# Performance work log

Hardware: AMD Instinct MI355X
Metric: run time of the kernel (lower is better)

The kernel has to match this reference:

```python
import jax, jax.numpy as jnp
import numpy as np

NUM_EXPERTS = 8
TOP_K = 2
D_MODEL = 1024
D_MLP = 3584
BATCH, POS = 2, 2048


def setup_inputs() -> dict:
    key = jax.random.key(0)
    ks = jax.random.split(key, 5)
    scale = 0.02
    x = jax.random.normal(ks[0], (BATCH, POS, D_MODEL), dtype=jnp.float32)
    W_gate = jax.random.normal(ks[1], (NUM_EXPERTS, D_MODEL), dtype=jnp.float32) * scale
    W1 = jax.random.normal(ks[2], (NUM_EXPERTS, D_MLP, D_MODEL), dtype=jnp.float32) * scale
    W3 = jax.random.normal(ks[3], (NUM_EXPERTS, D_MLP, D_MODEL), dtype=jnp.float32) * scale
    W2 = jax.random.normal(ks[4], (NUM_EXPERTS, D_MODEL, D_MLP), dtype=jnp.float32) * scale
    return {"x": x, "W_gate": W_gate, "W1": W1, "W3": W3, "W2": W2}


def reference(x, W_gate, W1, W3, W2):
    batch, pos, d_model = x.shape
    xt = x.reshape(-1, d_model)                      # [T, d]
    T = xt.shape[0]

    # --- top-2 softmax gating ---
    gate_logits = xt @ W_gate.T                      # [T, E]
    weights = jax.nn.softmax(gate_logits.astype(jnp.float32), axis=-1)
    top_w, top_i = jax.lax.top_k(weights, TOP_K)     # [T, k]
    top_w = top_w / jnp.sum(top_w, axis=-1, keepdims=True)
    top_w = top_w.astype(gate_logits.dtype)

    # dense combine weights: zero for non-selected experts  [T, E]
    combine = jnp.zeros((T, NUM_EXPERTS), dtype=xt.dtype)
    combine = combine.at[jnp.arange(T)[:, None], top_i].set(top_w)

    # --- per-expert SwiGLU MLP, computed dense over all tokens ---
    h1 = jnp.einsum('td,efd->etf', xt, W1)           # [E, T, ffn]
    h3 = jnp.einsum('td,efd->etf', xt, W3)           # [E, T, ffn]
    h = jax.nn.silu(h1) * h3                         # [E, T, ffn]
    expert_out = jnp.einsum('etf,edf->etd', h, W2)   # [E, T, d]

    # --- weighted combine ---
    out = jnp.einsum('etd,te->td', expert_out, combine)  # [T, d]
    return out.reshape(batch, pos, d_model)
```

## Files before the change

### kernel.cpp

```cpp
#include <hip/hip_runtime.h>
#include <hip/hip_bf16.h>
#include <math.h>


#define NUM_EXPERTS 8
#define TOPK 2
#define D_MODEL 1024
#define D_MLP 3584
#define T_TOKENS 4096
#define NSLOT (T_TOKENS * TOPK)
#define SLOT_CAP 9216

#define BM 128
#define BN 128
#define BK 32
#define LDT 40

typedef __attribute__((ext_vector_type(8))) short bf16x8;
typedef __attribute__((ext_vector_type(4))) float f32x4;

#define WS_SMALL 147456
#define H_BYTES ((size_t)SLOT_CAP * D_MLP * 2)
#define XB_OFF (WS_SMALL + H_BYTES)
#define XB_BYTES ((size_t)T_TOKENS * D_MODEL * 2)
#define W1B_OFF (XB_OFF + XB_BYTES)
#define W13_BYTES ((size_t)NUM_EXPERTS * (size_t)D_MLP * D_MODEL * 2)
#define W3B_OFF (W1B_OFF + W13_BYTES)
#define WS_FULL (W3B_OFF + W13_BYTES)
#define WS_NEEDED_OLD (WS_SMALL + H_BYTES)

__device__ inline unsigned short f32_to_bf16(float f) {
  union { float f; unsigned int u; } v; v.f = f;
  unsigned int u = v.u;
  unsigned int r = (u + 0x7FFFu + ((u >> 16) & 1u)) >> 16;
  return (unsigned short)r;
}

__device__ inline bf16x8 pack8(float4 a, float4 b) {
  bf16x8 v;
  v[0] = (short)f32_to_bf16(a.x); v[1] = (short)f32_to_bf16(a.y);
  v[2] = (short)f32_to_bf16(a.z); v[3] = (short)f32_to_bf16(a.w);
  v[4] = (short)f32_to_bf16(b.x); v[5] = (short)f32_to_bf16(b.y);
  v[6] = (short)f32_to_bf16(b.z); v[7] = (short)f32_to_bf16(b.w);
  return v;
}

__device__ __forceinline__ void gload16(const void* g, void* l) {
  __builtin_amdgcn_global_load_lds(
      (__attribute__((address_space(1))) void*)g,
      (__attribute__((address_space(3))) void*)l, 16, 0, 0);
}

__global__ void zero_kernel(float4* __restrict__ p, int n4) {
  int i = blockIdx.x * blockDim.x + threadIdx.x;
  if (i < n4) p[i] = make_float4(0.f, 0.f, 0.f, 0.f);
}

__global__ __launch_bounds__(256) void cvt_kernel(const float* __restrict__ src,
                                                  unsigned short* __restrict__ dst,
                                                  int n8) {
  int i = blockIdx.x * blockDim.x + threadIdx.x;
  const int stride = gridDim.x * blockDim.x;
  for (; i < n8; i += stride) {
    const float4* s = (const float4*)(src + (size_t)i * 8);
    float4 a = s[0], b = s[1];
    *(bf16x8*)(dst + (size_t)i * 8) = pack8(a, b);
  }
}

__global__ __launch_bounds__(64) void gate_kernel(const float* __restrict__ x,
                            const float* __restrict__ Wg,
                            int* __restrict__ top_idx,
                            float* __restrict__ top_w) {
  const int t = blockIdx.x;
  const int lane = threadIdx.x;
  const float* xr = x + (size_t)t * D_MODEL;

  float xs[16];
#pragma unroll
  for (int i = 0; i < 16; ++i) xs[i] = xr[lane + i * 64];

  float logits[NUM_EXPERTS];
#pragma unroll
  for (int e = 0; e < NUM_EXPERTS; ++e) {
    const float* wr = Wg + (size_t)e * D_MODEL;
    float s = 0.f;
#pragma unroll
    for (int i = 0; i < 16; ++i) s += xs[i] * wr[lane + i * 64];
    for (int o = 32; o > 0; o >>= 1) s += __shfl_down(s, o);
    logits[e] = s;
  }

  if (lane == 0) {
    int i0 = 0;
#pragma unroll
    for (int e = 1; e < NUM_EXPERTS; ++e)
      if (logits[e] > logits[i0]) i0 = e;
    int i1 = -1;
#pragma unroll
    for (int e = 0; e < NUM_EXPERTS; ++e) {
      if (e == i0) continue;
      if (i1 < 0 || logits[e] > logits[i1]) i1 = e;
    }
    float w0 = 1.0f / (1.0f + expf(logits[i1] - logits[i0]));
    top_idx[2 * t] = i0; top_idx[2 * t + 1] = i1;
    top_w[2 * t] = w0;   top_w[2 * t + 1] = 1.0f - w0;
  }
}

__global__ __launch_bounds__(256) void route_kernel(int* __restrict__ top_idx,
                             const float* __restrict__ top_w,
                             int* __restrict__ hdr,
                             int* __restrict__ slot_token,
                             float* __restrict__ slot_weight) {
  __shared__ int cnt[NUM_EXPERTS];
  __shared__ int off[NUM_EXPERTS];
  __shared__ int cur[NUM_EXPERTS];
  const int tid = threadIdx.x;
  if (tid < NUM_EXPERTS) cnt[tid] = 0;
  __syncthreads();
  for (int k = tid; k < NSLOT; k += 256) atomicAdd(&cnt[top_idx[k]], 1);
  __syncthreads();
  if (tid == 0) {
    int o = 0;
    for (int e = 0; e < NUM_EXPERTS; ++e) {
      off[e] = o;
      int p = (cnt[e] + BM - 1) & ~(BM - 1);
      hdr[e] = cnt[e];
      hdr[8 + e] = o;
      hdr[16 + e] = p;
      o += p;
    }
  }
  __syncthreads();
  if (tid < NUM_EXPERTS) cur[tid] = off[tid];
  for (int i = tid; i < SLOT_CAP; i += 256) { slot_token[i] = 0; slot_weight[i] = 0.0f; }
  __syncthreads();
  for (int k = tid; k < NSLOT; k += 256) {
    int e = top_idx[k];
    int p = atomicAdd(&cur[e], 1);
    slot_token[p] = k >> 1;
    slot_weight[p] = top_w[k];
    top_idx[k] = p;
  }
}

__global__ __launch_bounds__(256) void gemm1_p(
    const unsigned short* __restrict__ Xb,
    const unsigned short* __restrict__ W1b,
    const unsigned short* __restrict__ W3b,
    const int* __restrict__ hdr,
    const int* __restrict__ slot_token,
    unsigned short* __restrict__ H) {
  const int e = blockIdx.z;
  const int pad_cnt = hdr[16 + e];
  const int m0 = blockIdx.y * BM;
  if (m0 >= pad_cnt) return;
  const int base = hdr[8 + e];
  const int n0 = blockIdx.x * BN;

  __shared__ unsigned short As[2][BM * BK];
  __shared__ unsigned short B1s[2][BN * BK];
  __shared__ unsigned short B3s[2][BN * BK];

  const int tid = threadIdx.x;
  const int lane = tid & 63;
  const int wave = tid >> 6;
  const int wm = (wave >> 1) * 64;
  const int wn = (wave & 1) * 64;
  const int l15 = lane & 15;
  const int quad = lane >> 4;

  const int r0 = tid >> 2;
  const int cc = (tid & 3) * 8;
  const int tokA0 = slot_token[base + m0 + r0];
  const int tokA1 = slot_token[base + m0 + 64 + r0];
  const unsigned short* gA0 = Xb + (size_t)tokA0 * D_MODEL + cc;
  const unsigned short* gA1 = Xb + (size_t)tokA1 * D_MODEL + cc;
  const unsigned short* gB1_0 = W1b + ((size_t)e * D_MLP + n0 + r0) * D_MODEL + cc;
  const unsigned short* gB1_1 = gB1_0 + (size_t)64 * D_MODEL;
  const unsigned short* gB3_0 = W3b + ((size_t)e * D_MLP + n0 + r0) * D_MODEL + cc;
  const unsigned short* gB3_1 = gB3_0 + (size_t)64 * D_MODEL;
  const int wb = wave * 512;

  const f32x4 fzero = {0.f, 0.f, 0.f, 0.f};
  f32x4 acc1[4][4], acc3[4][4];
#pragma unroll
  for (int i = 0; i < 4; ++i)
#pragma unroll
    for (int j = 0; j < 4; ++j) { acc1[i][j] = fzero; acc3[i][j] = fzero; }

#define NT1 (D_MODEL / BK)
  gload16(gA0, &As[0][wb]);
  gload16(gA1, &As[0][2048 + wb]);
  gload16(gB1_0, &B1s[0][wb]);
  gload16(gB1_1, &B1s[0][2048 + wb]);
  gload16(gB3_0, &B3s[0][wb]);
  gload16(gB3_1, &B3s[0][2048 + wb]);

#pragma unroll
  for (int t = 0; t < NT1; ++t) {
    const int p = t & 1;
    if (t + 1 < NT1) {
      const int q = (t + 1) & 1;
      const int k1 = (t + 1) * BK;
      gload16(gA0 + k1, &As[q][wb]);
      gload16(gA1 + k1, &As[q][2048 + wb]);
      gload16(gB1_0 + k1, &B1s[q][wb]);
      gload16(gB1_1 + k1, &B1s[q][2048 + wb]);
      gload16(gB3_0 + k1, &B3s[q][wb]);
      gload16(gB3_1 + k1, &B3s[q][2048 + wb]);
      asm volatile("s_waitcnt vmcnt(6)" ::: "memory");
    } else {
      asm volatile("s_waitcnt vmcnt(0)" ::: "memory");
    }
    __builtin_amdgcn_s_barrier();
    asm volatile("" ::: "memory");

    bf16x8 af[4], b1f[4], b3f[4];
#pragma unroll
    for (int i = 0; i < 4; ++i)
      af[i] = *(const bf16x8*)(&As[p][(wm + i * 16 + l15) * BK + quad * 8]);
#pragma unroll
    for (int j = 0; j < 4; ++j) {
      b1f[j] = *(const bf16x8*)(&B1s[p][(wn + j * 16 + l15) * BK + quad * 8]);
      b3f[j] = *(const bf16x8*)(&B3s[p][(wn + j * 16 + l15) * BK + quad * 8]);
    }
#pragma unroll
    for (int i = 0; i < 4; ++i)
#pragma unroll
      for (int j = 0; j < 4; ++j) {
        acc1[i][j] = __builtin_amdgcn_mfma_f32_16x16x32_bf16(af[i], b1f[j], acc1[i][j], 0, 0, 0);
        acc3[i][j] = __builtin_amdgcn_mfma_f32_16x16x32_bf16(af[i], b3f[j], acc3[i][j], 0, 0, 0);
      }
    asm volatile("" ::: "memory");
    __builtin_amdgcn_s_barrier();
  }

  const size_t hbase = (size_t)(base + m0);
#pragma unroll
  for (int i = 0; i < 4; ++i) {
    const int mrow = wm + i * 16 + quad * 4;
#pragma unroll
    for (int r = 0; r < 4; ++r) {
      unsigned short* hrow = H + (hbase + mrow + r) * D_MLP + n0;
#pragma unroll
      for (int j = 0; j < 4; ++j) {
        float h1 = acc1[i][j][r];
        float h3 = acc3[i][j][r];
        float s = h1 / (1.0f + __expf(-h1));
        hrow[wn + j * 16 + l15] = f32_to_bf16(s * h3);
      }
    }
  }
}

__global__ __launch_bounds__(256) void gemm2_p(
    const unsigned short* __restrict__ H,
    const unsigned short* __restrict__ W2b,
    const int* __restrict__ hdr,
    float* __restrict__ Y) {
  const int e = blockIdx.z;
  const int pad_cnt = hdr[16 + e];
  const int m0 = blockIdx.y * BM;
  if (m0 >= pad_cnt) return;
  const int base = hdr[8 + e];
  const int n0 = blockIdx.x * BN;

  __shared__ unsigned short As[2][BM * BK];
  __shared__ unsigned short Bs[2][BN * BK];

  const int tid = threadIdx.x;
  const int lane = tid & 63;
  const int wave = tid >> 6;
  const int wm = (wave >> 1) * 64;
  const int wn = (wave & 1) * 64;
  const int l15 = lane & 15;
  const int quad = lane >> 4;

  const int r0 = tid >> 2;
  const int cc = (tid & 3) * 8;
  const unsigned short* gA0 = H + (size_t)(base + m0 + r0) * D_MLP + cc;
  const unsigned short* gA1 = gA0 + (size_t)64 * D_MLP;
  const unsigned short* gB0 = W2b + ((size_t)e * D_MODEL + n0 + r0) * D_MLP + cc;
  const unsigned short* gB1 = gB0 + (size_t)64 * D_MLP;
  const int wb = wave * 512;

  const f32x4 fzero = {0.f, 0.f, 0.f, 0.f};
  f32x4 acc[4][4];
#pragma unroll
  for (int i = 0; i < 4; ++i)
#pragma unroll
    for (int j = 0; j < 4; ++j) acc[i][j] = fzero;

#define NT2 (D_MLP / BK)
  gload16(gA0, &As[0][wb]);
  gload16(gA1, &As[0][2048 + wb]);
  gload16(gB0, &Bs[0][wb]);
  gload16(gB1, &Bs[0][2048 + wb]);

#pragma unroll 2
  for (int t = 0; t < NT2; ++t) {
    const int p = t & 1;
    if (t + 1 < NT2) {
      const int q = (t + 1) & 1;
      const int k1 = (t + 1) * BK;
      gload16(gA0 + k1, &As[q][wb]);
      gload16(gA1 + k1, &As[q][2048 + wb]);
      gload16(gB0 + k1, &Bs[q][wb]);
      gload16(gB1 + k1, &Bs[q][2048 + wb]);
      asm volatile("s_waitcnt vmcnt(4)" ::: "memory");
    } else {
      asm volatile("s_waitcnt vmcnt(0)" ::: "memory");
    }
    __builtin_amdgcn_s_barrier();
    asm volatile("" ::: "memory");

    bf16x8 af[4], bf[4];
#pragma unroll
    for (int i = 0; i < 4; ++i)
      af[i] = *(const bf16x8*)(&As[p][(wm + i * 16 + l15) * BK + quad * 8]);
#pragma unroll
    for (int j = 0; j < 4; ++j)
      bf[j] = *(const bf16x8*)(&Bs[p][(wn + j * 16 + l15) * BK + quad * 8]);
#pragma unroll
    for (int i = 0; i < 4; ++i)
#pragma unroll
      for (int j = 0; j < 4; ++j)
        acc[i][j] = __builtin_amdgcn_mfma_f32_16x16x32_bf16(af[i], bf[j], acc[i][j], 0, 0, 0);
    asm volatile("" ::: "memory");
    __builtin_amdgcn_s_barrier();
  }

#pragma unroll
  for (int i = 0; i < 4; ++i) {
    const int mrow = wm + i * 16 + quad * 4;
#pragma unroll
    for (int r = 0; r < 4; ++r) {
      float* yrow = Y + (size_t)(base + m0 + mrow + r) * D_MODEL + n0;
#pragma unroll
      for (int j = 0; j < 4; ++j)
        yrow[wn + j * 16 + l15] = acc[i][j][r];
    }
  }
}

__global__ __launch_bounds__(256) void combine_kernel(
    const float* __restrict__ Y,
    const int* __restrict__ slot_of,
    const float* __restrict__ top_w,
    float* __restrict__ out) {
  const int t = blockIdx.x;
  const int c = threadIdx.x;
  const int p0 = slot_of[2 * t], p1 = slot_of[2 * t + 1];
  const float w0 = top_w[2 * t], w1 = top_w[2 * t + 1];
  const float4 y0 = ((const float4*)(Y + (size_t)p0 * D_MODEL))[c];
  const float4 y1 = ((const float4*)(Y + (size_t)p1 * D_MODEL))[c];
  float4 o;
  o.x = w0 * y0.x + w1 * y1.x;
  o.y = w0 * y0.y + w1 * y1.y;
  o.z = w0 * y0.z + w1 * y1.z;
  o.w = w0 * y0.w + w1 * y1.w;
  ((float4*)(out + (size_t)t * D_MODEL))[c] = o;
}


__global__ __launch_bounds__(256) void gemm1_kernel(const float* __restrict__ x,
                             const float* __restrict__ W1,
                             const float* __restrict__ W3,
                             const int* __restrict__ hdr,
                             const int* __restrict__ slot_token,
                             unsigned short* __restrict__ H) {
  const int e = blockIdx.z;
  const int pad_cnt = hdr[16 + e];
  const int m0 = blockIdx.y * BM;
  if (m0 >= pad_cnt) return;
  const int base = hdr[8 + e];
  const int n0 = blockIdx.x * BN;

  __shared__ unsigned short As[BM * LDT];
  __shared__ unsigned short B1s[BN * LDT];
  __shared__ unsigned short B3s[BN * LDT];

  const int tid = threadIdx.x;
  const int lane = tid & 63;
  const int wave = tid >> 6;
  const int wm = (wave >> 1) * 64;
  const int wn = (wave & 1) * 64;
  const int l15 = lane & 15;
  const int quad = lane >> 4;

  const int sr = tid >> 1;
  const int sc = (tid & 1) * 16;
  const float* arow = x + (size_t)slot_token[base + m0 + sr] * D_MODEL + sc;
  const float* b1row = W1 + ((size_t)e * D_MLP + n0 + sr) * D_MODEL + sc;
  const float* b3row = W3 + ((size_t)e * D_MLP + n0 + sr) * D_MODEL + sc;

  const f32x4 fzero = {0.f, 0.f, 0.f, 0.f};
  f32x4 acc1[4][4], acc3[4][4];
#pragma unroll
  for (int i = 0; i < 4; ++i)
#pragma unroll
    for (int j = 0; j < 4; ++j) { acc1[i][j] = fzero; acc3[i][j] = fzero; }

  for (int k0 = 0; k0 < D_MODEL; k0 += BK) {
    const float4* ap = (const float4*)(arow + k0);
    const float4* b1p = (const float4*)(b1row + k0);
    const float4* b3p = (const float4*)(b3row + k0);
    float4 a0 = ap[0], a1 = ap[1], a2 = ap[2], a3 = ap[3];
    float4 c0 = b1p[0], c1 = b1p[1], c2 = b1p[2], c3 = b1p[3];
    float4 d0 = b3p[0], d1 = b3p[1], d2 = b3p[2], d3 = b3p[3];
    __syncthreads();
    *(bf16x8*)(&As[sr * LDT + sc]) = pack8(a0, a1);
    *(bf16x8*)(&As[sr * LDT + sc + 8]) = pack8(a2, a3);
    *(bf16x8*)(&B1s[sr * LDT + sc]) = pack8(c0, c1);
    *(bf16x8*)(&B1s[sr * LDT + sc + 8]) = pack8(c2, c3);
    *(bf16x8*)(&B3s[sr * LDT + sc]) = pack8(d0, d1);
    *(bf16x8*)(&B3s[sr * LDT + sc + 8]) = pack8(d2, d3);
    __syncthreads();

    bf16x8 a_frag[4], b1_frag[4], b3_frag[4];
#pragma unroll
    for (int i = 0; i < 4; ++i)
      a_frag[i] = *(const bf16x8*)(&As[(wm + i * 16 + l15) * LDT + quad * 8]);
#pragma unroll
    for (int j = 0; j < 4; ++j) {
      b1_frag[j] = *(const bf16x8*)(&B1s[(wn + j * 16 + l15) * LDT + quad * 8]);
      b3_frag[j] = *(const bf16x8*)(&B3s[(wn + j * 16 + l15) * LDT + quad * 8]);
    }
#pragma unroll
    for (int i = 0; i < 4; ++i)
#pragma unroll
      for (int j = 0; j < 4; ++j) {
        acc1[i][j] = __builtin_amdgcn_mfma_f32_16x16x32_bf16(a_frag[i], b1_frag[j], acc1[i][j], 0, 0, 0);
        acc3[i][j] = __builtin_amdgcn_mfma_f32_16x16x32_bf16(a_frag[i], b3_frag[j], acc3[i][j], 0, 0, 0);
      }
  }

  const size_t hbase = (size_t)(base + m0);
#pragma unroll
  for (int i = 0; i < 4; ++i) {
    const int mrow = wm + i * 16 + quad * 4;
#pragma unroll
    for (int r = 0; r < 4; ++r) {
      unsigned short* hrow = H + (hbase + mrow + r) * D_MLP + n0;
#pragma unroll
      for (int j = 0; j < 4; ++j) {
        float h1 = acc1[i][j][r];
        float h3 = acc3[i][j][r];
        float s = h1 / (1.0f + __expf(-h1));
        hrow[wn + j * 16 + l15] = f32_to_bf16(s * h3);
      }
    }
  }
}

__global__ __launch_bounds__(256) void gemm2_kernel(const unsigned short* __restrict__ H,
                             const float* __restrict__ W2,
                             const int* __restrict__ hdr,
                             const int* __restrict__ slot_token,
                             const float* __restrict__ slot_weight,
                             float* __restrict__ out) {
  const int e = blockIdx.z;
  const int pad_cnt = hdr[16 + e];
  const int m0 = blockIdx.y * BM;
  if (m0 >= pad_cnt) return;
  const int base = hdr[8 + e];
  const int n0 = blockIdx.x * BN;

  __shared__ unsigned short As[BM * LDT];
  __shared__ unsigned short Bs[BN * LDT];

  const int tid = threadIdx.x;
  const int lane = tid & 63;
  const int wave = tid >> 6;
  const int wm = (wave >> 1) * 64;
  const int wn = (wave & 1) * 64;
  const int l15 = lane & 15;
  const int quad = lane >> 4;

  const int sr = tid >> 1;
  const int sc = (tid & 1) * 16;
  const unsigned short* arow = H + (size_t)(base + m0 + sr) * D_MLP + sc;
  const float* brow = W2 + ((size_t)e * D_MODEL + n0 + sr) * D_MLP + sc;

  const f32x4 fzero = {0.f, 0.f, 0.f, 0.f};
  f32x4 acc[4][4];
#pragma unroll
  for (int i = 0; i < 4; ++i)
#pragma unroll
    for (int j = 0; j < 4; ++j) acc[i][j] = fzero;

  for (int k0 = 0; k0 < D_MLP; k0 += BK) {
    const uint4* ap = (const uint4*)(arow + k0);
    uint4 a0 = ap[0], a1 = ap[1];
    const float4* bp = (const float4*)(brow + k0);
    float4 c0 = bp[0], c1 = bp[1], c2 = bp[2], c3 = bp[3];
    __syncthreads();
    *(uint4*)(&As[sr * LDT + sc]) = a0;
    *(uint4*)(&As[sr * LDT + sc + 8]) = a1;
    *(bf16x8*)(&Bs[sr * LDT + sc]) = pack8(c0, c1);
    *(bf16x8*)(&Bs[sr * LDT + sc + 8]) = pack8(c2, c3);
    __syncthreads();

    bf16x8 a_frag[4], b_frag[4];
#pragma unroll
    for (int i = 0; i < 4; ++i)
      a_frag[i] = *(const bf16x8*)(&As[(wm + i * 16 + l15) * LDT + quad * 8]);
#pragma unroll
    for (int j = 0; j < 4; ++j)
      b_frag[j] = *(const bf16x8*)(&Bs[(wn + j * 16 + l15) * LDT + quad * 8]);
#pragma unroll
    for (int i = 0; i < 4; ++i)
#pragma unroll
      for (int j = 0; j < 4; ++j)
        acc[i][j] = __builtin_amdgcn_mfma_f32_16x16x32_bf16(a_frag[i], b_frag[j], acc[i][j], 0, 0, 0);
  }

#pragma unroll
  for (int i = 0; i < 4; ++i) {
    const int mrow = wm + i * 16 + quad * 4;
#pragma unroll
    for (int r = 0; r < 4; ++r) {
      const int srow = base + m0 + mrow + r;
      const float w = slot_weight[srow];
      if (w != 0.0f) {
        const int tok = slot_token[srow];
        float* orow = out + (size_t)tok * D_MODEL + n0;
#pragma unroll
        for (int j = 0; j < 4; ++j)
          atomicAdd(&orow[wn + j * 16 + l15], acc[i][j][r] * w);
      }
    }
  }
}

extern "C" void kernel_launch(void* const* d_in, const int* in_sizes, int n_in,
                              void* d_out, int out_size, void* d_ws, size_t ws_size,
                              hipStream_t stream) {
  const float* x  = (const float*)d_in[0];
  const float* Wg = (const float*)d_in[1];
  const float* W1 = (const float*)d_in[2];
  const float* W3 = (const float*)d_in[3];
  const float* W2 = (const float*)d_in[4];
  float* out = (float*)d_out;

  if (ws_size < WS_NEEDED_OLD) return;

  char* ws = (char*)d_ws;
  int*   top_idx     = (int*)(ws);
  float* top_w       = (float*)(ws + 32768);
  int*   hdr         = (int*)(ws + 65536);
  int*   slot_token  = (int*)(ws + 65792);
  float* slot_weight = (float*)(ws + 102656);
  unsigned short* H  = (unsigned short*)(ws + WS_SMALL);

  gate_kernel<<<T_TOKENS, 64, 0, stream>>>(x, Wg, top_idx, top_w);
  route_kernel<<<1, 256, 0, stream>>>(top_idx, top_w, hdr, slot_token, slot_weight);

  if (ws_size >= WS_FULL) {
    unsigned short* Xb  = (unsigned short*)(ws + XB_OFF);
    unsigned short* W1b = (unsigned short*)(ws + W1B_OFF);
    unsigned short* W3b = (unsigned short*)(ws + W3B_OFF);
    unsigned short* W2b = W1b;
    float* Y = (float*)(ws + W3B_OFF);

    cvt_kernel<<<2048, 256, 0, stream>>>(x, Xb, T_TOKENS * D_MODEL / 8);
    cvt_kernel<<<2048, 256, 0, stream>>>(W1, W1b, NUM_EXPERTS * D_MLP * D_MODEL / 8);
    cvt_kernel<<<2048, 256, 0, stream>>>(W3, W3b, NUM_EXPERTS * D_MLP * D_MODEL / 8);
    gemm1_p<<<dim3(D_MLP / BN, T_TOKENS / BM, NUM_EXPERTS), 256, 0, stream>>>(
        Xb, W1b, W3b, hdr, slot_token, H);
    cvt_kernel<<<2048, 256, 0, stream>>>(W2, W2b, NUM_EXPERTS * D_MODEL * D_MLP / 8);
    gemm2_p<<<dim3(D_MODEL / BN, T_TOKENS / BM, NUM_EXPERTS), 256, 0, stream>>>(
        H, W2b, hdr, Y);
    combine_kernel<<<T_TOKENS, 256, 0, stream>>>(Y, top_idx, top_w, out);
  } else {
    zero_kernel<<<(out_size / 4 + 255) / 256, 256, 0, stream>>>((float4*)d_out, out_size / 4);
    gemm1_kernel<<<dim3(D_MLP / BN, T_TOKENS / BM, NUM_EXPERTS), 256, 0, stream>>>(
        x, W1, W3, hdr, slot_token, H);
    gemm2_kernel<<<dim3(D_MODEL / BN, T_TOKENS / BM, NUM_EXPERTS), 256, 0, stream>>>(
        H, W2, hdr, slot_token, slot_weight, out);
  }
}
```

Before: 644.1 us.

## Fold weight conversions into gate/route/gemm1 launches and single-sync GEMM pipeline

Converts x to bf16 inside the gate kernel and runs the W1/W3 conversion in extra blocks of the routing kernel. When workspace allows, W2 conversion runs as an extra z-slice of gemm1, overlapping with expert GEMM work. The GEMM main loops move to one waitcnt plus barrier per K step after compute instead of waiting before compute. The aim is fewer launches and overlapping conversion bandwidth with compute. In exchange, the routing block shares the GPU with heavy conversion blocks, and the gemm1 W2 slice needs a larger workspace to be used.

Measured after the change: 711.8 us. +10.5%, slower.

```diff
diff --git a/kernel.cpp b/kernel.cpp
--- a/kernel.cpp
+++ b/kernel.cpp
@@ -27,7 +27,11 @@
 #define W13_BYTES ((size_t)NUM_EXPERTS * (size_t)D_MLP * D_MODEL * 2)
 #define W3B_OFF (W1B_OFF + W13_BYTES)
 #define WS_FULL (W3B_OFF + W13_BYTES)
+#define W2B_OFF WS_FULL
+#define WS_BIG (W2B_OFF + W13_BYTES)
 #define WS_NEEDED_OLD (WS_SMALL + H_BYTES)
+
+#define NW8 (NUM_EXPERTS * D_MLP * D_MODEL / 8)
 
 __device__ inline unsigned short f32_to_bf16(float f) {
   union { float f; unsigned int u; } v; v.f = f;
@@ -71,7 +75,8 @@
 __global__ __launch_bounds__(64) void gate_kernel(const float* __restrict__ x,
                             const float* __restrict__ Wg,
                             int* __restrict__ top_idx,
-                            float* __restrict__ top_w) {
+                            float* __restrict__ top_w,
+                            unsigned short* __restrict__ Xb) {
   const int t = blockIdx.x;
   const int lane = threadIdx.x;
   const float* xr = x + (size_t)t * D_MODEL;
@@ -80,6 +85,14 @@
 #pragma unroll
   for (int i = 0; i < 16; ++i) xs[i] = xr[lane + i * 64];
 
+  if (Xb) {
+    const float4* xr4 = (const float4*)(xr + lane * 16);
+    float4 a0 = xr4[0], a1 = xr4[1], a2 = xr4[2], a3 = xr4[3];
+    unsigned short* xbrow = Xb + (size_t)t * D_MODEL + lane * 16;
+    *(bf16x8*)(xbrow) = pack8(a0, a1);
+    *(bf16x8*)(xbrow + 8) = pack8(a2, a3);
+  }
+
   float logits[NUM_EXPERTS];
 #pragma unroll
   for (int e = 0; e < NUM_EXPERTS; ++e) {
@@ -108,15 +121,35 @@
   }
 }
 
-__global__ __launch_bounds__(256) void route_kernel(int* __restrict__ top_idx,
-                             const float* __restrict__ top_w,
-                             int* __restrict__ hdr,
-                             int* __restrict__ slot_token,
-                             float* __restrict__ slot_weight) {
+__global__ __launch_bounds__(256) void route_cvt_kernel(
+    int* __restrict__ top_idx,
+    const float* __restrict__ top_w,
+    int* __restrict__ hdr,
+    int* __restrict__ slot_token,
+    float* __restrict__ slot_weight,
+    const float* __restrict__ W1,
+    const float* __restrict__ W3,
+    unsigned short* __restrict__ W1b,
+    unsigned short* __restrict__ W3b) {
+  const int tid = threadIdx.x;
+  if (blockIdx.x != 0) {
+    const int wid = blockIdx.x - 1;
+    const int stride = (gridDim.x - 1) * 256;
+    for (int i = wid * 256 + tid; i < NW8; i += stride) {
+      const float4* s = (const float4*)(W1 + (size_t)i * 8);
+      float4 a = s[0], b = s[1];
+      *(bf16x8*)(W1b + (size_t)i * 8) = pack8(a, b);
+    }
+    for (int i = wid * 256 + tid; i < NW8; i += stride) {
+      const float4* s = (const float4*)(W3 + (size_t)i * 8);
+      float4 a = s[0], b = s[1];
+      *(bf16x8*)(W3b + (size_t)i * 8) = pack8(a, b);
+    }
+    return;
+  }
   __shared__ int cnt[NUM_EXPERTS];
   __shared__ int off[NUM_EXPERTS];
   __shared__ int cur[NUM_EXPERTS];
-  const int tid = threadIdx.x;
   if (tid < NUM_EXPERTS) cnt[tid] = 0;
   __syncthreads();
   for (int k = tid; k < NSLOT; k += 256) atomicAdd(&cnt[top_idx[k]], 1);
@@ -151,7 +184,19 @@
     const unsigned short* __restrict__ W3b,
     const int* __restrict__ hdr,
     const int* __restrict__ slot_token,
-    unsigned short* __restrict__ H) {
+    unsigned short* __restrict__ H,
+    const float* __restrict__ W2src,
+    unsigned short* __restrict__ W2dst) {
+  if (blockIdx.z == NUM_EXPERTS) {
+    const int wid = blockIdx.y * gridDim.x + blockIdx.x;
+    const int stride = gridDim.x * gridDim.y * 256;
+    for (int i = wid * 256 + threadIdx.x; i < NW8; i += stride) {
+      const float4* s = (const float4*)(W2src + (size_t)i * 8);
+      float4 a = s[0], b = s[1];
+      *(bf16x8*)(W2dst + (size_t)i * 8) = pack8(a, b);
+    }
+    return;
+  }
   const int e = blockIdx.z;
   const int pad_cnt = hdr[16 + e];
   const int m0 = blockIdx.y * BM;
@@ -197,12 +242,15 @@
   gload16(gB1_1, &B1s[0][2048 + wb]);
   gload16(gB3_0, &B3s[0][wb]);
   gload16(gB3_1, &B3s[0][2048 + wb]);
+  asm volatile("s_waitcnt vmcnt(0)" ::: "memory");
+  __builtin_amdgcn_s_barrier();
+  asm volatile("" ::: "memory");
 
 #pragma unroll
   for (int t = 0; t < NT1; ++t) {
     const int p = t & 1;
     if (t + 1 < NT1) {
-      const int q = (t + 1) & 1;
+      const int q = p ^ 1;
       const int k1 = (t + 1) * BK;
       gload16(gA0 + k1, &As[q][wb]);
       gload16(gA1 + k1, &As[q][2048 + wb]);
@@ -210,13 +258,7 @@
       gload16(gB1_1 + k1, &B1s[q][2048 + wb]);
       gload16(gB3_0 + k1, &B3s[q][wb]);
       gload16(gB3_1 + k1, &B3s[q][2048 + wb]);
-      asm volatile("s_waitcnt vmcnt(6)" ::: "memory");
-    } else {
-      asm volatile("s_waitcnt vmcnt(0)" ::: "memory");
-    }
-    __builtin_amdgcn_s_barrier();
-    asm volatile("" ::: "memory");
-
+    }
     bf16x8 af[4], b1f[4], b3f[4];
 #pragma unroll
     for (int i = 0; i < 4; ++i)
@@ -233,8 +275,11 @@
         acc1[i][j] = __builtin_amdgcn_mfma_f32_16x16x32_bf16(af[i], b1f[j], acc1[i][j], 0, 0, 0);
         acc3[i][j] = __builtin_amdgcn_mfma_f32_16x16x32_bf16(af[i], b3f[j], acc3[i][j], 0, 0, 0);
       }
-    asm volatile("" ::: "memory");
-    __builtin_amdgcn_s_barrier();
+    if (t + 1 < NT1) {
+      asm volatile("s_waitcnt vmcnt(0)" ::: "memory");
+      __builtin_amdgcn_s_barrier();
+      asm volatile("" ::: "memory");
+    }
   }
 
   const size_t hbase = (size_t)(base + m0);
@@ -298,24 +343,21 @@
   gload16(gA1, &As[0][2048 + wb]);
   gload16(gB0, &Bs[0][wb]);
   gload16(gB1, &Bs[0][2048 + wb]);
+  asm volatile("s_waitcnt vmcnt(0)" ::: "memory");
+  __builtin_amdgcn_s_barrier();
+  asm volatile("" ::: "memory");
 
 #pragma unroll 2
   for (int t = 0; t < NT2; ++t) {
     const int p = t & 1;
     if (t + 1 < NT2) {
-      const int q = (t + 1) & 1;
+      const int q = p ^ 1;
       const int k1 = (t + 1) * BK;
       gload16(gA0 + k1, &As[q][wb]);
       gload16(gA1 + k1, &As[q][2048 + wb]);
       gload16(gB0 + k1, &Bs[q][wb]);
       gload16(gB1 + k1, &Bs[q][2048 + wb]);
-      asm volatile("s_waitcnt vmcnt(4)" ::: "memory");
-    } else {
-      asm volatile("s_waitcnt vmcnt(0)" ::: "memory");
-    }
-    __builtin_amdgcn_s_barrier();
-    asm volatile("" ::: "memory");
-
+    }
     bf16x8 af[4], bf[4];
 #pragma unroll
     for (int i = 0; i < 4; ++i)
@@ -328,8 +370,11 @@
 #pragma unroll
       for (int j = 0; j < 4; ++j)
         acc[i][j] = __builtin_amdgcn_mfma_f32_16x16x32_bf16(af[i], bf[j], acc[i][j], 0, 0, 0);
-    asm volatile("" ::: "memory");
-    __builtin_amdgcn_s_barrier();
+    if (t + 1 < NT2) {
+      asm volatile("s_waitcnt vmcnt(0)" ::: "memory");
+      __builtin_amdgcn_s_barrier();
+      asm volatile("" ::: "memory");
+    }
   }
 
 #pragma unroll
@@ -555,26 +600,34 @@
   float* slot_weight = (float*)(ws + 102656);
   unsigned short* H  = (unsigned short*)(ws + WS_SMALL);
 
-  gate_kernel<<<T_TOKENS, 64, 0, stream>>>(x, Wg, top_idx, top_w);
-  route_kernel<<<1, 256, 0, stream>>>(top_idx, top_w, hdr, slot_token, slot_weight);
-
   if (ws_size >= WS_FULL) {
     unsigned short* Xb  = (unsigned short*)(ws + XB_OFF);
     unsigned short* W1b = (unsigned short*)(ws + W1B_OFF);
     unsigned short* W3b = (unsigned short*)(ws + W3B_OFF);
-    unsigned short* W2b = W1b;
     float* Y = (float*)(ws + W3B_OFF);
-
-    cvt_kernel<<<2048, 256, 0, stream>>>(x, Xb, T_TOKENS * D_MODEL / 8);
-    cvt_kernel<<<2048, 256, 0, stream>>>(W1, W1b, NUM_EXPERTS * D_MLP * D_MODEL / 8);
-    cvt_kernel<<<2048, 256, 0, stream>>>(W3, W3b, NUM_EXPERTS * D_MLP * D_MODEL / 8);
-    gemm1_p<<<dim3(D_MLP / BN, T_TOKENS / BM, NUM_EXPERTS), 256, 0, stream>>>(
-        Xb, W1b, W3b, hdr, slot_token, H);
-    cvt_kernel<<<2048, 256, 0, stream>>>(W2, W2b, NUM_EXPERTS * D_MODEL * D_MLP / 8);
+    const bool big = (ws_size >= WS_BIG);
+    unsigned short* W2b = big ? (unsigned short*)(ws + W2B_OFF)
+                              : W1b;
+
+    gate_kernel<<<T_TOKENS, 64, 0, stream>>>(x, Wg, top_idx, top_w, Xb);
+    route_cvt_kernel<<<2049, 256, 0, stream>>>(top_idx, top_w, hdr, slot_token,
+                                               slot_weight, W1, W3, W1b, W3b);
+    if (big) {
+      gemm1_p<<<dim3(D_MLP / BN, T_TOKENS / BM, NUM_EXPERTS + 1), 256, 0, stream>>>(
+          Xb, W1b, W3b, hdr, slot_token, H, W2, W2b);
+    } else {
+      gemm1_p<<<dim3(D_MLP / BN, T_TOKENS / BM, NUM_EXPERTS), 256, 0, stream>>>(
+          Xb, W1b, W3b, hdr, slot_token, H, nullptr, nullptr);
+      cvt_kernel<<<2048, 256, 0, stream>>>(W2, W2b, NW8);
+    }
     gemm2_p<<<dim3(D_MODEL / BN, T_TOKENS / BM, NUM_EXPERTS), 256, 0, stream>>>(
         H, W2b, hdr, Y);
     combine_kernel<<<T_TOKENS, 256, 0, stream>>>(Y, top_idx, top_w, out);
   } else {
+    gate_kernel<<<T_TOKENS, 64, 0, stream>>>(x, Wg, top_idx, top_w, nullptr);
+    route_cvt_kernel<<<1, 256, 0, stream>>>(top_idx, top_w, hdr, slot_token,
+                                            slot_weight, nullptr, nullptr,
+                                            nullptr, nullptr);
     zero_kernel<<<(out_size / 4 + 255) / 256, 256, 0, stream>>>((float4*)d_out, out_size / 4);
     gemm1_kernel<<<dim3(D_MLP / BN, T_TOKENS / BM, NUM_EXPERTS), 256, 0, stream>>>(
         x, W1, W3, hdr, slot_token, H);
```
